# Optimization experiments

Measured on AMD Instinct MI355X. Metric: run time of the kernel, lower is better.

The kernel has to match this reference:

```python
import jax, jax.numpy as jnp
import numpy as np

M, L = 256, 256
E_EDGES = L - 1
EPS = 1e-12
HX, HZ, JZ = 3.0, 0.25, -1.0


def setup_inputs() -> dict:
    key = jax.random.key(0)
    k1, k2 = jax.random.split(key, 2)
    # original: uniform(-pi/2, pi/2); narrowed to keep cos(theta_m - theta_b) away from 0
    theta = jax.random.uniform(k1, (M, L), minval=-0.3, maxval=0.3, dtype=jnp.float32)
    coef = jax.random.uniform(k2, (M,), minval=-1.0, maxval=1.0, dtype=jnp.float32)
    edges_u = jnp.arange(E_EDGES, dtype=jnp.int32)       # 1D chain
    edges_v = edges_u + 1
    strengths = jnp.ones((E_EDGES,), dtype=jnp.float32)
    return {"theta": theta, "coef": coef, "edges_u": edges_u,
            "edges_v": edges_v, "strengths": strengths}


def reference(theta, coef, edges_u, edges_v, strengths):
    # theta: [M, L], coef: [M]
    cos_m = jnp.cos(theta)
    sin_m = jnp.sin(theta)
    cm = cos_m[:, None, :]   # [M,1,L] -> row m
    sm = sin_m[:, None, :]
    cb = cos_m[None, :, :]   # [1,M,L] -> row b
    sb = sin_m[None, :, :]
    # pairwise angle-sum/difference trig, all [M, M, L]
    cosd = cm * cb + sm * sb            # cos(theta_m - theta_b)
    sind = sm * cb - cm * sb            # sin(theta_m - theta_b)
    sins = sm * cb + cm * sb            # sin(theta_m + theta_b)
    coss = cm * cb - sm * sb            # cos(theta_m + theta_b)
    inv = 1.0 / (cosd + EPS)

    P = jnp.prod(cosd, axis=-1)                     # [M,M] overlap products
    U = jnp.sum(sins * inv, axis=-1)                # [M,M] sigma_x amplitude ratios
    V = jnp.sum(coss * inv, axis=-1)                # [M,M] sigma_z amplitude ratios
    a = coss * inv                                  # [M,M,L] per-site z ratio

    # ZZ interaction over graph edges
    Szz = jnp.einsum('e,mbe->mb', strengths,
                     a[:, :, edges_u] * a[:, :, edges_v])  # [M,M]

    F_total = HZ * V + HX * U + JZ * Szz            # [M,M]
    base = coef[:, None] * coef[None, :] * P        # [M,M]
    N = jnp.sum(base * F_total)
    D = jnp.sum(base)

    cP = coef[None, :] * P                          # c_b * P
    dN_dc = 2.0 * jnp.sum(cP * F_total, axis=1)     # [M]
    dD_dc = 2.0 * jnp.sum(cP, axis=1)               # [M]

    g_d = -sind * inv                               # d log cosd / d theta_mq
    Gxz = (-HZ * sins + HX * coss) * inv + (HZ * coss + HX * sins) * (sind * inv * inv)

    # incident-edge neighbor sums: inc[m,b,q] = sum_{e incident to q} s_e * a[m,b,nbr]
    uu = jnp.concatenate([edges_u, edges_v])
    vv = jnp.concatenate([edges_v, edges_u])
    ss = jnp.concatenate([strengths, strengths])
    inc = jnp.zeros_like(a).at[:, :, uu].add(ss * a[:, :, vv])
    Gzz = (-sins * inv + coss * (sind * inv * inv)) * inc * JZ

    w = base[:, :, None]                            # [M,M,1]
    dD_dtheta = 2.0 * jnp.sum(w * g_d, axis=1)      # [M,L]
    dN_dtheta = 2.0 * jnp.sum(
        w * (g_d * F_total[:, :, None] + Gxz + Gzz), axis=1)  # [M,L]

    E = N / D
    dE_dc = (dN_dc - E * dD_dc) / D
    dE_dtheta = (dN_dtheta - E * dD_dtheta) / D
    return dE_dtheta, dE_dc, E / L
```

## Files before the change

### kernel.cpp

```cpp
#include <hip/hip_runtime.h>
#include <math.h>

#define HXc 3.0f
#define HZc 0.25f

#define OFF_TANR 0
#define OFF_F    65536
#define OFF_CP   131072
#define OFF_NM   196608
#define OFF_DM   196864
#define OFF_CN   197120
#define OFF_CD   197376

__device__ __forceinline__ float tan_poly(float x) {
    float y = x * x;
    float p = fmaf(y, 62.0f / 2835.0f, 17.0f / 315.0f);
    p = fmaf(y, p, 2.0f / 15.0f);
    p = fmaf(y, p, 1.0f / 3.0f);
    return x * fmaf(y, p, 1.0f);
}

__device__ __forceinline__ float cos_poly(float x) {
    float y = x * x;
    float p = fmaf(y, 1.0f / 40320.0f, -1.0f / 720.0f);
    p = fmaf(y, p, 1.0f / 24.0f);
    p = fmaf(y, p, -0.5f);
    return fmaf(y, p, 1.0f);
}

__global__ __launch_bounds__(512) void k_fwd(
        const float* __restrict__ theta,
        const float* __restrict__ coef,
        const float* __restrict__ strengths,
        float* __restrict__ ws) {
    int m = blockIdx.x, tid = threadIdx.x;
    __shared__ float tmL[256], sLDS[256], Flds[256], cPlds[256];
    __shared__ float prp[4];
    __shared__ float red[32][4];

    if (tid < 256) {
        float x = theta[m * 256 + tid];
        float tn = tan_poly(x);
        tmL[tid] = tn;
        ws[OFF_TANR + m * 256 + tid] = tn;
        sLDS[tid] = (tid < 255) ? strengths[tid] : 0.0f;
        float pr = cos_poly(x);
        for (int o = 32; o; o >>= 1) pr *= __shfl_xor(pr, o);
        if ((tid & 63) == 0) prp[tid >> 6] = pr;
    }
    __syncthreads();
    float Cpm = prp[0] * prp[1] * prp[2] * prp[3];
    float coefm = coef[m];

    int w = tid >> 6, lane = tid & 63;
    int sw = lane >> 4, sl = lane & 15;
    int l0 = sl * 16;

    float tm[16], sLv[16];
#pragma unroll
    for (int j = 0; j < 16; ++j) {
        tm[j] = tmL[l0 + j];
        int lm1 = l0 + j - 1;
        sLv[j] = (lm1 >= 0) ? sLDS[lm1] : 0.0f;
    }

    float nA = 0.f, dA = 0.f, cNA = 0.f, cDA = 0.f;
    for (int r = 0; r < 8; ++r) {
        int b = r * 32 + w * 4 + sw;
        const float4* thp = (const float4*)&theta[b * 256 + l0];
        float4 t0 = thp[0], t1 = thp[1], t2 = thp[2], t3 = thp[3];
        float th[16] = {t0.x, t0.y, t0.z, t0.w, t1.x, t1.y, t1.z, t1.w,
                        t2.x, t2.y, t2.z, t2.w, t3.x, t3.y, t3.z, t3.w};
        float pl = 1.f, ul = 0.f, vl = 0.f, zl = 0.f;
        float a_prev = 0.f, a_first = 0.f;
#pragma unroll
        for (int j = 0; j < 16; ++j) {
            float tb = tan_poly(th[j]);
            float cb = cos_poly(th[j]);
            float qq = tm[j] * tb;
            float w1 = 1.0f + qq;
            float inv = __builtin_amdgcn_rcpf(w1);
            pl *= cb * w1;
            ul = fmaf(tm[j] + tb, inv, ul);
            float a = fmaf(-qq, inv, inv);
            vl += a;
            if (j == 0) a_first = a;
            else        zl = fmaf(sLv[j] * a_prev, a, zl);
            a_prev = a;
        }
        float aP = __shfl_up(a_prev, 1);
        float sB = (sl == 0) ? 0.0f : sLv[0];
        zl = fmaf(sB * aP, a_first, zl);
#pragma unroll
        for (int o = 1; o < 16; o <<= 1) {
            pl *= __shfl_xor(pl, o);
            ul += __shfl_xor(ul, o);
            vl += __shfl_xor(vl, o);
            zl += __shfl_xor(zl, o);
        }
        float P = Cpm * pl;
        float F = fmaf(HZc, vl, fmaf(HXc, ul, -zl));
        float cP = coef[b] * P;
        if (sl == 0) { Flds[b] = F; cPlds[b] = cP; }
        float base = coefm * cP;
        dA += base;
        nA = fmaf(base, F, nA);
        cDA += cP;
        cNA = fmaf(cP, F, cNA);
    }
    if (sl == 0) {
        int s = w * 4 + sw;
        red[s][0] = nA; red[s][1] = dA; red[s][2] = cNA; red[s][3] = cDA;
    }
    __syncthreads();
    if (tid < 256) {
        ws[OFF_F + m * 256 + tid] = Flds[tid];
        ws[OFF_CP + m * 256 + tid] = cPlds[tid];
    }
    if (tid < 32) {
        float v0 = red[tid][0], v1 = red[tid][1];
        float v2 = red[tid][2], v3 = red[tid][3];
#pragma unroll
        for (int o = 1; o < 32; o <<= 1) {
            v0 += __shfl_xor(v0, o);
            v1 += __shfl_xor(v1, o);
            v2 += __shfl_xor(v2, o);
            v3 += __shfl_xor(v3, o);
        }
        if (tid == 0) {
            ws[OFF_NM + m] = v0; ws[OFF_DM + m] = v1;
            ws[OFF_CN + m] = v2; ws[OFF_CD + m] = v3;
        }
    }
}

__global__ __launch_bounds__(512) void k_grad(
        const float* __restrict__ coef,
        const float* __restrict__ strengths,
        const float* __restrict__ ws,
        float* __restrict__ out) {
    int m = blockIdx.x, tid = threadIdx.x;
    const float* __restrict__ tanR = ws + OFF_TANR;
    __shared__ float sLDS[256], Flds[256], cPlds[256];
    __shared__ float gN[8 * 256], gD[8 * 256];
    __shared__ float rn[4], rd[4];

    if (tid < 256) {
        sLDS[tid] = (tid < 255) ? strengths[tid] : 0.0f;
        Flds[tid] = ws[OFF_F + m * 256 + tid];
        cPlds[tid] = ws[OFF_CP + m * 256 + tid];
        float nv = ws[OFF_NM + tid], dv = ws[OFF_DM + tid];
        for (int o = 32; o; o >>= 1) {
            nv += __shfl_xor(nv, o);
            dv += __shfl_xor(dv, o);
        }
        if ((tid & 63) == 0) { rn[tid >> 6] = nv; rd[tid >> 6] = dv; }
    }
    __syncthreads();
    float N = rn[0] + rn[1] + rn[2] + rn[3];
    float D = rd[0] + rd[1] + rd[2] + rd[3];
    float E = N / D;
    float invD = 1.0f / D;
    float s2 = 2.0f * invD;

    {
        int w = tid >> 6, lane = tid & 63;
        int l0 = lane * 4;
        float coefm = coef[m];
        float4 tm4 = *(const float4*)&tanR[m * 256 + l0];
        float tm[4] = {tm4.x, tm4.y, tm4.z, tm4.w};
        float tm2[4] = {2.0f * tm4.x, 2.0f * tm4.y, 2.0f * tm4.z, 2.0f * tm4.w};
        float sR[4], sL[4];
#pragma unroll
        for (int j = 0; j < 4; ++j) {
            int l = l0 + j;
            sR[j] = sLDS[l];
            sL[j] = (l > 0) ? sLDS[l - 1] : 0.0f;
        }
        float pN[4] = {0.f, 0.f, 0.f, 0.f};
        float pD[4] = {0.f, 0.f, 0.f, 0.f};

        for (int i = 0; i < 32; ++i) {
            int b = w * 32 + i;
            float4 tb4 = *(const float4*)&tanR[b * 256 + l0];
            float tb[4] = {tb4.x, tb4.y, tb4.z, tb4.w};
            float Fv = Flds[b];
            float base = coefm * cPlds[b];

            float A[4], S[4], G[4];
#pragma unroll
            for (int j = 0; j < 4; ++j) {
                float qq = tm[j] * tb[j];
                float w1 = 1.0f + qq;
                float inv = __builtin_amdgcn_rcpf(w1);
                G[j] = (tm[j] - tb[j]) * inv;
                S[j] = fmaf(tm2[j], inv, -G[j]);
                A[j] = fmaf(-qq, inv, inv);
            }
            float aLn = __shfl_up(A[3], 1);
            if (lane == 0) aLn = 0.0f;
            float aRn = __shfl_down(A[0], 1);
            if (lane == 63) aRn = 0.0f;
            float am1[4] = {aLn, A[0], A[1], A[2]};
            float ap1[4] = {A[1], A[2], A[3], aRn};
#pragma unroll
            for (int j = 0; j < 4; ++j) {
                float Gxz = fmaf(HXc, A[j], -HZc * S[j])
                          + fmaf(HZc, A[j], HXc * S[j]) * G[j];
                float K = fmaf(-A[j], G[j], S[j]);
                float inc = fmaf(sR[j], ap1[j], sL[j] * am1[j]);
                float term = fmaf(K, inc, Gxz);
                term = fmaf(-Fv, G[j], term);
                pN[j] = fmaf(base, term, pN[j]);
                pD[j] = fmaf(-base, G[j], pD[j]);
            }
        }
        ((float4*)gN)[w * 64 + lane] = make_float4(pN[0], pN[1], pN[2], pN[3]);
        ((float4*)gD)[w * 64 + lane] = make_float4(pD[0], pD[1], pD[2], pD[3]);
    }
    __syncthreads();
    if (tid < 256) {
        float sn = 0.0f, sd = 0.0f;
#pragma unroll
        for (int ww = 0; ww < 8; ++ww) {
            sn += gN[ww * 256 + tid];
            sd += gD[ww * 256 + tid];
        }
        out[m * 256 + tid] = s2 * (sn - E * sd);
    }
    if (tid == 0)
        out[65536 + m] = s2 * (ws[OFF_CN + m] - E * ws[OFF_CD + m]);
    if (m == 0 && tid == 1)
        out[65792] = E * (1.0f / 256.0f);
}

extern "C" void kernel_launch(void* const* d_in, const int* in_sizes, int n_in,
                              void* d_out, int out_size, void* d_ws, size_t ws_size,
                              hipStream_t stream) {
    const float* theta = (const float*)d_in[0];
    const float* coef = (const float*)d_in[1];
    const float* strengths = (const float*)d_in[4];
    float* out = (float*)d_out;
    float* ws = (float*)d_ws;

    k_fwd<<<256, 512, 0, stream>>>(theta, coef, strengths, ws);
    k_grad<<<256, 512, 0, stream>>>(coef, strengths, ws, out);
}
```

Baseline: 91.42 us.

## Stage tan(theta_b) tiles in LDS and derive cos via rsqrt in forward kernel

The forward kernel now computes tan(theta_b) cooperatively into a padded 64x257 LDS tile for each group of 64 b rows. Each thread then sweeps 32 sites of one b row from LDS instead of loading theta and evaluating both tan and cos polynomials per element. cos is derived as rsqrt(1+tan^2), which removes the cos polynomial. Per-row partial sums are reduced through an LDS float4 array rather than 16-lane shuffles. This adds barriers per tile and a serial 64-thread reduction step, and uses a much larger LDS footprint that may cut occupancy.

```diff
diff --git a/kernel.cpp b/kernel.cpp
--- a/kernel.cpp
+++ b/kernel.cpp
@@ -20,23 +20,17 @@
     return x * fmaf(y, p, 1.0f);
 }
 
-__device__ __forceinline__ float cos_poly(float x) {
-    float y = x * x;
-    float p = fmaf(y, 1.0f / 40320.0f, -1.0f / 720.0f);
-    p = fmaf(y, p, 1.0f / 24.0f);
-    p = fmaf(y, p, -0.5f);
-    return fmaf(y, p, 1.0f);
-}
-
 __global__ __launch_bounds__(512) void k_fwd(
         const float* __restrict__ theta,
         const float* __restrict__ coef,
         const float* __restrict__ strengths,
         float* __restrict__ ws) {
     int m = blockIdx.x, tid = threadIdx.x;
-    __shared__ float tmL[256], sLDS[256], Flds[256], cPlds[256];
+    __shared__ float tanB[64][257];
+    __shared__ float tmL[256], sLDS[256];
+    __shared__ float Flds[256], cPlds[256];
+    __shared__ float4 red[8][64];
     __shared__ float prp[4];
-    __shared__ float red[32][4];
 
     if (tid < 256) {
         float x = theta[m * 256 + tid];
@@ -44,92 +38,90 @@
         tmL[tid] = tn;
         ws[OFF_TANR + m * 256 + tid] = tn;
         sLDS[tid] = (tid < 255) ? strengths[tid] : 0.0f;
-        float pr = cos_poly(x);
-        for (int o = 32; o; o >>= 1) pr *= __shfl_xor(pr, o);
-        if ((tid & 63) == 0) prp[tid >> 6] = pr;
+        float cm = rsqrtf(fmaf(tn, tn, 1.0f));
+        for (int o = 32; o; o >>= 1) cm *= __shfl_xor(cm, o);
+        if ((tid & 63) == 0) prp[tid >> 6] = cm;
     }
     __syncthreads();
     float Cpm = prp[0] * prp[1] * prp[2] * prp[3];
     float coefm = coef[m];
 
-    int w = tid >> 6, lane = tid & 63;
-    int sw = lane >> 4, sl = lane & 15;
-    int l0 = sl * 16;
-
-    float tm[16], sLv[16];
-#pragma unroll
-    for (int j = 0; j < 16; ++j) {
-        tm[j] = tmL[l0 + j];
-        int lm1 = l0 + j - 1;
-        sLv[j] = (lm1 >= 0) ? sLDS[lm1] : 0.0f;
-    }
-
+    int c = tid & 255, rp = tid >> 8;
+    int bL = tid & 63, w = tid >> 6;
+    int l0 = w * 32;
     float nA = 0.f, dA = 0.f, cNA = 0.f, cDA = 0.f;
-    for (int r = 0; r < 8; ++r) {
-        int b = r * 32 + w * 4 + sw;
-        const float4* thp = (const float4*)&theta[b * 256 + l0];
-        float4 t0 = thp[0], t1 = thp[1], t2 = thp[2], t3 = thp[3];
-        float th[16] = {t0.x, t0.y, t0.z, t0.w, t1.x, t1.y, t1.z, t1.w,
-                        t2.x, t2.y, t2.z, t2.w, t3.x, t3.y, t3.z, t3.w};
-        float pl = 1.f, ul = 0.f, vl = 0.f, zl = 0.f;
-        float a_prev = 0.f, a_first = 0.f;
-#pragma unroll
-        for (int j = 0; j < 16; ++j) {
-            float tb = tan_poly(th[j]);
-            float cb = cos_poly(th[j]);
-            float qq = tm[j] * tb;
-            float w1 = 1.0f + qq;
+
+    for (int t = 0; t < 4; ++t) {
+        int b0 = t * 64;
+#pragma unroll
+        for (int k = 0; k < 32; ++k) {
+            int r = 2 * k + rp;
+            tanB[r][c] = tan_poly(theta[(b0 + r) * 256 + c]);
+        }
+        __syncthreads();
+        float p = 1.f, u = 0.f, v = 0.f, z = 0.f, a_prev = 0.f;
+        if (l0 > 0) {
+            float tb = tanB[bL][l0 - 1];
+            float q = tmL[l0 - 1] * tb;
+            float inv = __builtin_amdgcn_rcpf(1.0f + q);
+            a_prev = fmaf(-q, inv, inv);
+        }
+#pragma unroll
+        for (int j = 0; j < 32; ++j) {
+            int l = l0 + j;
+            float tb = tanB[bL][l];
+            float tm = tmL[l];
+            float q = tm * tb;
+            float w1 = 1.0f + q;
             float inv = __builtin_amdgcn_rcpf(w1);
-            pl *= cb * w1;
-            ul = fmaf(tm[j] + tb, inv, ul);
-            float a = fmaf(-qq, inv, inv);
-            vl += a;
-            if (j == 0) a_first = a;
-            else        zl = fmaf(sLv[j] * a_prev, a, zl);
+            float cb = rsqrtf(fmaf(tb, tb, 1.0f));
+            p *= cb * w1;
+            u = fmaf(tm + tb, inv, u);
+            float a = fmaf(-q, inv, inv);
+            v += a;
+            float sPrev = (l > 0) ? sLDS[l - 1] : 0.0f;
+            z = fmaf(sPrev * a_prev, a, z);
             a_prev = a;
         }
-        float aP = __shfl_up(a_prev, 1);
-        float sB = (sl == 0) ? 0.0f : sLv[0];
-        zl = fmaf(sB * aP, a_first, zl);
-#pragma unroll
-        for (int o = 1; o < 16; o <<= 1) {
-            pl *= __shfl_xor(pl, o);
-            ul += __shfl_xor(ul, o);
-            vl += __shfl_xor(vl, o);
-            zl += __shfl_xor(zl, o);
-        }
-        float P = Cpm * pl;
-        float F = fmaf(HZc, vl, fmaf(HXc, ul, -zl));
-        float cP = coef[b] * P;
-        if (sl == 0) { Flds[b] = F; cPlds[b] = cP; }
-        float base = coefm * cP;
-        dA += base;
-        nA = fmaf(base, F, nA);
-        cDA += cP;
-        cNA = fmaf(cP, F, cNA);
-    }
-    if (sl == 0) {
-        int s = w * 4 + sw;
-        red[s][0] = nA; red[s][1] = dA; red[s][2] = cNA; red[s][3] = cDA;
+        red[w][bL] = make_float4(p, u, v, z);
+        __syncthreads();
+        if (tid < 64) {
+            int b = b0 + tid;
+            float4 r0 = red[0][tid], r1 = red[1][tid];
+            float4 r2 = red[2][tid], r3 = red[3][tid];
+            float4 r4 = red[4][tid], r5 = red[5][tid];
+            float4 r6 = red[6][tid], r7 = red[7][tid];
+            float P = Cpm * (((r0.x * r1.x) * (r2.x * r3.x)) *
+                             ((r4.x * r5.x) * (r6.x * r7.x)));
+            float U = ((r0.y + r1.y) + (r2.y + r3.y)) + ((r4.y + r5.y) + (r6.y + r7.y));
+            float V = ((r0.z + r1.z) + (r2.z + r3.z)) + ((r4.z + r5.z) + (r6.z + r7.z));
+            float Z = ((r0.w + r1.w) + (r2.w + r3.w)) + ((r4.w + r5.w) + (r6.w + r7.w));
+            float F = fmaf(HZc, V, fmaf(HXc, U, -Z));
+            float cP = coef[b] * P;
+            Flds[b] = F;
+            cPlds[b] = cP;
+            float base = coefm * cP;
+            dA += base;
+            nA = fmaf(base, F, nA);
+            cDA += cP;
+            cNA = fmaf(cP, F, cNA);
+        }
     }
     __syncthreads();
     if (tid < 256) {
         ws[OFF_F + m * 256 + tid] = Flds[tid];
         ws[OFF_CP + m * 256 + tid] = cPlds[tid];
     }
-    if (tid < 32) {
-        float v0 = red[tid][0], v1 = red[tid][1];
-        float v2 = red[tid][2], v3 = red[tid][3];
-#pragma unroll
-        for (int o = 1; o < 32; o <<= 1) {
-            v0 += __shfl_xor(v0, o);
-            v1 += __shfl_xor(v1, o);
-            v2 += __shfl_xor(v2, o);
-            v3 += __shfl_xor(v3, o);
+    if (tid < 64) {
+        for (int o = 1; o < 64; o <<= 1) {
+            nA += __shfl_xor(nA, o);
+            dA += __shfl_xor(dA, o);
+            cNA += __shfl_xor(cNA, o);
+            cDA += __shfl_xor(cDA, o);
         }
         if (tid == 0) {
-            ws[OFF_NM + m] = v0; ws[OFF_DM + m] = v1;
-            ws[OFF_CN + m] = v2; ws[OFF_CD + m] = v3;
+            ws[OFF_NM + m] = nA;  ws[OFF_DM + m] = dA;
+            ws[OFF_CN + m] = cNA; ws[OFF_CD + m] = cDA;
         }
     }
 }
```

Measured after the change: 94.06 us. 2.9% more time.
